# Optimization experiments

Hardware: AMD Instinct MI355X
Metric: run time of the kernel (lower is better)

## Reference

```python
import jax, jax.numpy as jnp
import numpy as np

IN_FEATURES = 4096
OUT_FEATURES = 11008
BATCH = 16


def setup_inputs() -> dict:
    key = jax.random.key(0)
    k1, k2, k3 = jax.random.split(key, 3)
    x = jax.random.normal(k1, (BATCH, IN_FEATURES), dtype=jnp.float32)
    # int8 quantized weight codes, stored as int32 in [0,255] then shifted to [-128,127]
    w_q = jax.random.randint(k2, (OUT_FEATURES, IN_FEATURES), 0, 255, dtype=jnp.int32)
    # per-tensor quantization scale (max(|w|)/127 in the original; any positive scalar here)
    scale = jnp.ones((1,), dtype=jnp.float32) * 0.01
    bias = jax.random.normal(k3, (OUT_FEATURES,), dtype=jnp.float32)
    return {"x": x, "w_q": w_q, "scale": scale, "bias": bias}


def reference(x, w_q, scale, bias):
    # Codec decode is lossless on the int8 codes; math-relevant part is
    # dequantize (codes * scale) followed by F.linear(x, W, b).
    codes = w_q.astype(jnp.float32) - 128.0  # shift to signed int8 range
    weight = codes * scale[0]                 # [out_features, in_features]
    return x @ weight.T + bias                # [batch, out_features]
```

## Files before the change

kernel.cpp:

```cpp
#include <hip/hip_runtime.h>
#include <stdint.h>


constexpr int IN_F  = 4096;
constexpr int OUT_F = 11008;
constexpr int NWAVES = 8;
constexpr int BK = 512;
constexpr int NCHUNK = IN_F / BK;
constexpr int ROW_BYTES = BK * 4;
constexpr int CHUNK_BYTES = 16 * ROW_BYTES;

typedef _Float16 f16x8 __attribute__((ext_vector_type(8)));
typedef float    f32x4 __attribute__((ext_vector_type(4)));

__device__ inline f16x8 cvt_codes(int4 a, int4 b) {
    f16x8 r;
    r[0] = (_Float16)(a.x - 128); r[1] = (_Float16)(a.y - 128);
    r[2] = (_Float16)(a.z - 128); r[3] = (_Float16)(a.w - 128);
    r[4] = (_Float16)(b.x - 128); r[5] = (_Float16)(b.y - 128);
    r[6] = (_Float16)(b.z - 128); r[7] = (_Float16)(b.w - 128);
    return r;
}

__global__ __launch_bounds__(NWAVES * 64, 4)
void qlinear_mfma(const float* __restrict__ x,
                  const int*   __restrict__ wq,
                  const float* __restrict__ scale,
                  const float* __restrict__ bias,
                  float*       __restrict__ out)
{
    __shared__ __align__(16) char smem[2 * CHUNK_BYTES];
    __shared__ f32x4 red[NWAVES][64];

    const int tid  = threadIdx.x;
    const int lane = tid & 63;
    const int wave = tid >> 6;
    const int obase = blockIdx.x * 16;

    const int ncol = lane & 15;
    const int kgrp = lane >> 4;

    f16x8 a[2 * NCHUNK];
    {
        const float* xp = x + (size_t)ncol * IN_F;
        #pragma unroll
        for (int f = 0; f < 2 * NCHUNK; ++f) {
            const int c  = f >> 1, jj = f & 1;
            const int kb = c * BK + (wave * 2 + jj) * 32 + kgrp * 8;
            const float4 xa = *reinterpret_cast<const float4*>(xp + kb);
            const float4 xb = *reinterpret_cast<const float4*>(xp + kb + 4);
            f16x8 t;
            t[0] = (_Float16)xa.x; t[1] = (_Float16)xa.y;
            t[2] = (_Float16)xa.z; t[3] = (_Float16)xa.w;
            t[4] = (_Float16)xb.x; t[5] = (_Float16)xb.y;
            t[6] = (_Float16)xb.z; t[7] = (_Float16)xb.w;
            a[f] = t;
        }
    }

    const char* wq_bytes = reinterpret_cast<const char*>(wq);
    auto stage = [&](int c, int buf) {
        #pragma unroll
        for (int p = 0; p < 4; ++p) {
            const int row = p * 4 + (wave >> 1);
            const int within = (((wave & 1) * 1024) + lane * 16) ^ ((row & 7) << 4);
            const char* src = wq_bytes + (size_t)(obase + row) * (IN_F * 4)
                                       + (size_t)c * ROW_BYTES + within;
            char* dst = smem + buf * CHUNK_BYTES + p * 8192 + wave * 1024 + lane * 16;
            __builtin_amdgcn_global_load_lds(
                (const __attribute__((address_space(1))) void*)src,
                (__attribute__((address_space(3))) void*)dst, 16, 0, 0);
        }
    };

    stage(0, 0);
    __syncthreads();

    f32x4 acc = {0.f, 0.f, 0.f, 0.f};
    const int swz = (ncol & 7) << 4;

    for (int c = 0; c < NCHUNK; ++c) {
        const int buf = c & 1;
        if (c + 1 < NCHUNK) stage(c + 1, buf ^ 1);

        const char* rowbase = smem + buf * CHUNK_BYTES + ncol * ROW_BYTES;
        #pragma unroll
        for (int jj = 0; jj < 2; ++jj) {
            const int kb = wave * 2 + jj;
            const int lo = kgrp * 32 + kb * 128;
            const int4 w0 = *reinterpret_cast<const int4*>(rowbase + ((lo)      ^ swz));
            const int4 w1 = *reinterpret_cast<const int4*>(rowbase + ((lo + 16) ^ swz));
            const f16x8 bf = cvt_codes(w0, w1);
            acc = __builtin_amdgcn_mfma_f32_16x16x32_f16(a[c * 2 + jj], bf, acc, 0, 0, 0);
        }
        __syncthreads();
    }

    red[wave][lane] = acc;
    __syncthreads();

    if (wave == 0) {
        f32x4 s = red[0][lane];
        #pragma unroll
        for (int w = 1; w < NWAVES; ++w) s += red[w][lane];

        const float sc = scale[0];
        const float bo = bias[obase + ncol];
        const int   brow = kgrp * 4;
        #pragma unroll
        for (int r = 0; r < 4; ++r)
            out[(size_t)(brow + r) * OUT_F + obase + ncol] = s[r] * sc + bo;
    }
}

extern "C" void kernel_launch(void* const* d_in, const int* in_sizes, int n_in,
                              void* d_out, int out_size, void* d_ws, size_t ws_size,
                              hipStream_t stream) {
    const float* x     = (const float*)d_in[0];
    const int*   wq    = (const int*)d_in[1];
    const float* scale = (const float*)d_in[2];
    const float* bias  = (const float*)d_in[3];
    float*       out   = (float*)d_out;

    dim3 grid(OUT_F / 16);
    dim3 block(NWAVES * 64);
    qlinear_mfma<<<grid, block, 0, stream>>>(x, wq, scale, bias, out);
}
```

Before: 55.17 us.

## Use triple-buffered LDS pipeline with smaller chunks and vmcnt-based waits

Halves the K chunk size and switches from double to triple buffering, keeping two chunks of weight loads in flight. Per-iteration __syncthreads is replaced by explicit vmcnt waits plus s_barrier, and the K loop is fully unrolled. The aim is deeper overlap of the global-to-LDS weight streaming with compute, which matters because the kernel is bandwidth bound. The cost is twice as many barrier steps and removal of the occupancy hint from launch_bounds.

```diff
diff --git a/kernel.cpp b/kernel.cpp
--- a/kernel.cpp
+++ b/kernel.cpp
@@ -5,10 +5,11 @@
 constexpr int IN_F  = 4096;
 constexpr int OUT_F = 11008;
 constexpr int NWAVES = 8;
-constexpr int BK = 512;
+constexpr int BK     = 256;
 constexpr int NCHUNK = IN_F / BK;
-constexpr int ROW_BYTES = BK * 4;
-constexpr int CHUNK_BYTES = 16 * ROW_BYTES;
+constexpr int ROW_B  = BK * 4;
+constexpr int CH_B   = 16 * ROW_B;
+constexpr int NBUF   = 3;
 
 typedef _Float16 f16x8 __attribute__((ext_vector_type(8)));
 typedef float    f32x4 __attribute__((ext_vector_type(4)));
@@ -22,14 +23,14 @@
     return r;
 }
 
-__global__ __launch_bounds__(NWAVES * 64, 4)
+__global__ __launch_bounds__(NWAVES * 64)
 void qlinear_mfma(const float* __restrict__ x,
                   const int*   __restrict__ wq,
                   const float* __restrict__ scale,
                   const float* __restrict__ bias,
                   float*       __restrict__ out)
 {
-    __shared__ __align__(16) char smem[2 * CHUNK_BYTES];
+    __shared__ __align__(16) char smem[NBUF * CH_B];
     __shared__ f32x4 red[NWAVES][64];
 
     const int tid  = threadIdx.x;
@@ -40,60 +41,61 @@
     const int ncol = lane & 15;
     const int kgrp = lane >> 4;
 
-    f16x8 a[2 * NCHUNK];
+    f16x8 a[NCHUNK];
     {
-        const float* xp = x + (size_t)ncol * IN_F;
+        const float* xp = x + (size_t)ncol * IN_F + wave * 32 + kgrp * 8;
         #pragma unroll
-        for (int f = 0; f < 2 * NCHUNK; ++f) {
-            const int c  = f >> 1, jj = f & 1;
-            const int kb = c * BK + (wave * 2 + jj) * 32 + kgrp * 8;
-            const float4 xa = *reinterpret_cast<const float4*>(xp + kb);
-            const float4 xb = *reinterpret_cast<const float4*>(xp + kb + 4);
+        for (int c = 0; c < NCHUNK; ++c) {
+            const float4 xa = *reinterpret_cast<const float4*>(xp + c * BK);
+            const float4 xb = *reinterpret_cast<const float4*>(xp + c * BK + 4);
             f16x8 t;
             t[0] = (_Float16)xa.x; t[1] = (_Float16)xa.y;
             t[2] = (_Float16)xa.z; t[3] = (_Float16)xa.w;
             t[4] = (_Float16)xb.x; t[5] = (_Float16)xb.y;
             t[6] = (_Float16)xb.z; t[7] = (_Float16)xb.w;
-            a[f] = t;
+            a[c] = t;
         }
     }
 
     const char* wq_bytes = reinterpret_cast<const char*>(wq);
     auto stage = [&](int c, int buf) {
         #pragma unroll
-        for (int p = 0; p < 4; ++p) {
-            const int row = p * 4 + (wave >> 1);
-            const int within = (((wave & 1) * 1024) + lane * 16) ^ ((row & 7) << 4);
+        for (int p = 0; p < 2; ++p) {
+            const int row = wave * 2 + p;
+            const int within = (lane * 16) ^ ((row & 7) << 4);
             const char* src = wq_bytes + (size_t)(obase + row) * (IN_F * 4)
-                                       + (size_t)c * ROW_BYTES + within;
-            char* dst = smem + buf * CHUNK_BYTES + p * 8192 + wave * 1024 + lane * 16;
+                                       + (size_t)c * ROW_B + within;
+            char* dst = smem + buf * CH_B + row * ROW_B + lane * 16;
             __builtin_amdgcn_global_load_lds(
                 (const __attribute__((address_space(1))) void*)src,
                 (__attribute__((address_space(3))) void*)dst, 16, 0, 0);
         }
     };
 
+    asm volatile("s_waitcnt vmcnt(0)" ::: "memory");
+    __builtin_amdgcn_sched_barrier(0);
+
     stage(0, 0);
-    __syncthreads();
+    stage(1, 1);
 
     f32x4 acc = {0.f, 0.f, 0.f, 0.f};
     const int swz = (ncol & 7) << 4;
+    const int lo  = wave * 128 + kgrp * 32;
 
+    #pragma unroll
     for (int c = 0; c < NCHUNK; ++c) {
-        const int buf = c & 1;
-        if (c + 1 < NCHUNK) stage(c + 1, buf ^ 1);
+        if (c < NCHUNK - 1) asm volatile("s_waitcnt vmcnt(2)" ::: "memory");
+        else                asm volatile("s_waitcnt vmcnt(0)" ::: "memory");
+        __builtin_amdgcn_s_barrier();
+        __builtin_amdgcn_sched_barrier(0);
 
-        const char* rowbase = smem + buf * CHUNK_BYTES + ncol * ROW_BYTES;
-        #pragma unroll
-        for (int jj = 0; jj < 2; ++jj) {
-            const int kb = wave * 2 + jj;
-            const int lo = kgrp * 32 + kb * 128;
-            const int4 w0 = *reinterpret_cast<const int4*>(rowbase + ((lo)      ^ swz));
-            const int4 w1 = *reinterpret_cast<const int4*>(rowbase + ((lo + 16) ^ swz));
-            const f16x8 bf = cvt_codes(w0, w1);
-            acc = __builtin_amdgcn_mfma_f32_16x16x32_f16(a[c * 2 + jj], bf, acc, 0, 0, 0);
-        }
-        __syncthreads();
+        if (c + 2 < NCHUNK) stage(c + 2, (c + 2) % NBUF);
+
+        const char* rowbase = smem + (c % NBUF) * CH_B + ncol * ROW_B;
+        const int4 w0 = *reinterpret_cast<const int4*>(rowbase + ((lo)      ^ swz));
+        const int4 w1 = *reinterpret_cast<const int4*>(rowbase + ((lo + 16) ^ swz));
+        acc = __builtin_amdgcn_mfma_f32_16x16x32_f16(a[c], cvt_codes(w0, w1), acc, 0, 0, 0);
+        __builtin_amdgcn_sched_barrier(0);
     }
 
     red[wave][lane] = acc;
```

New measurement: 61.42 us. +11.3%, slower.
